# Kernel tuning notes

Hardware: AMD Instinct MI355X
Metric: run time of the kernel (lower is better)

The kernel has to match this reference:

```python
import jax, jax.numpy as jnp
import numpy as np

BOS_IDX = 1


def setup_inputs() -> dict:
    key = jax.random.key(0)
    ks = jax.random.split(key, 12)
    B, T, S, H, L, V = 16, 128, 64, 512, 2, 32000
    s = 0.05
    return {
        "encoder_outputs": jax.random.normal(ks[0], (B, S, H), jnp.float32),
        "encoder_h": jax.random.normal(ks[1], (L, B, H), jnp.float32) * s,
        "encoder_c": jax.random.normal(ks[2], (L, B, H), jnp.float32) * s,
        "target_tensor": jax.random.randint(ks[3], (B, T), 0, V),
        "embedding": jax.random.normal(ks[4], (V, H), jnp.float32) * s,
        "W_ih": jax.random.normal(ks[5], (L, 4 * H, H), jnp.float32) * s,
        "W_hh": jax.random.normal(ks[6], (L, 4 * H, H), jnp.float32) * s,
        "b_ih": jax.random.normal(ks[7], (L, 4 * H), jnp.float32) * s,
        "b_hh": jax.random.normal(ks[8], (L, 4 * H), jnp.float32) * s,
        "W_out": jax.random.normal(ks[9], (V, H), jnp.float32) * s,
        "b_out": jax.random.normal(ks[10], (V,), jnp.float32) * s,
    }


def reference(encoder_outputs, encoder_h, encoder_c, target_tensor,
              embedding, W_ih, W_hh, b_ih, b_hh, W_out, b_out):
    B, T = target_tensor.shape
    L = W_ih.shape[0]
    # Teacher-forced inputs: BOS then target[:, :-1]
    tokens = jnp.concatenate(
        [jnp.full((B, 1), BOS_IDX, dtype=target_tensor.dtype),
         target_tensor[:, :-1]], axis=1)  # [B, T]
    x = jax.nn.relu(embedding[tokens])  # [B, T, H]
    # The original loop resets (h, c) to encoder_states at EVERY step, so all
    # T single-step LSTM cells are independent -> vectorize over T.
    h_last, c_last = [], []
    for l in range(L):
        h0 = encoder_h[l]  # [B, H]
        c0 = encoder_c[l][:, None, :]  # [B, 1, H]
        gates = (jnp.einsum('bth,gh->btg', x, W_ih[l]) + b_ih[l]
                 + (jnp.einsum('bh,gh->bg', h0, W_hh[l]) + b_hh[l])[:, None, :])
        i, f, g, o = jnp.split(gates, 4, axis=-1)  # torch gate order i,f,g,o
        c = jax.nn.sigmoid(f) * c0 + jax.nn.sigmoid(i) * jnp.tanh(g)
        h = jax.nn.sigmoid(o) * jnp.tanh(c)  # [B, T, H]
        h_last.append(h[:, -1, :])
        c_last.append(c[:, -1, :])
        x = h  # input to next layer (dropout=0 / eval)
    logits = jnp.einsum('bth,vh->btv', x, W_out) + b_out  # [B, T, V]
    return logits, (jnp.stack(h_last), jnp.stack(c_last))
```

## Files before the change

### kernel.cpp

```cpp
#include <hip/hip_runtime.h>
#include <hip/hip_bf16.h>

typedef __bf16 bf16_t;
typedef __bf16 bf16x8 __attribute__((ext_vector_type(8)));
typedef __bf16 bf16x4 __attribute__((ext_vector_type(4)));
typedef float f32x4 __attribute__((ext_vector_type(4)));

#define B_ 16
#define T_ 128
#define H_ 512
#define L_ 2
#define V_ 32000
#define G_ 2048
#define M_ 2048

#define BN 128
#define BK 64

__device__ __forceinline__ float sigf(float x) { return 1.f / (1.f + __expf(-x)); }
__device__ __forceinline__ float tanhf_(float x) { return 2.f / (1.f + __expf(-2.f * x)) - 1.f; }


__global__ __launch_bounds__(256) void prep(const float* __restrict__ emb,
                                            const int* __restrict__ target,
                                            const float* __restrict__ enc_h,
                                            const float* __restrict__ W_ih,
                                            const float* __restrict__ W_hh,
                                            const float* __restrict__ b_ih,
                                            const float* __restrict__ b_hh,
                                            const float* __restrict__ W_out,
                                            bf16_t* __restrict__ x,
                                            bf16_t* __restrict__ wih_b,
                                            bf16_t* __restrict__ wout_b,
                                            float* __restrict__ biasall) {
    const int blk = blockIdx.x;
    const int tid = threadIdx.x;
    if (blk < 256) {
        int idx = blk * 256 + tid;
        int b = idx & 15;
        int c = (idx >> 4) & (G_ - 1);
        int l = idx >> 15;
        int gate = (c >> 4) & 3;
        int h = ((c >> 6) << 4) | (c & 15);
        int r = gate * H_ + h;
        const float* hrow = enc_h + ((size_t)l * B_ + b) * H_;
        const float* wrow = W_hh + ((size_t)l * G_ + r) * H_;
        float acc = b_ih[l * G_ + r] + b_hh[l * G_ + r];
        #pragma unroll 4
        for (int k = 0; k < H_; k += 4) {
            float4 hv = *(const float4*)(hrow + k);
            float4 wv = *(const float4*)(wrow + k);
            acc += hv.x * wv.x + hv.y * wv.y + hv.z * wv.z + hv.w * wv.w;
        }
        biasall[((size_t)l * B_ + b) * G_ + c] = acc;
    } else if (blk < 2304) {
        int idx = (blk - 256) * 256 + tid;
        int k4 = idx & 127;
        int c  = (idx >> 7) & (G_ - 1);
        int l  = idx >> 18;
        int gate = (c >> 4) & 3;
        int h = ((c >> 6) << 4) | (c & 15);
        int r = gate * H_ + h;
        float4 v = *(const float4*)(W_ih + ((size_t)l * G_ + r) * H_ + k4 * 4);
        bf16x4 o;
        o[0] = (bf16_t)v.x; o[1] = (bf16_t)v.y; o[2] = (bf16_t)v.z; o[3] = (bf16_t)v.w;
        *(bf16x4*)(wih_b + ((size_t)l * G_ + c) * H_ + k4 * 4) = o;
    } else if (blk < 3328) {
        int idx = (blk - 2304) * 256 + tid;
        int m  = idx >> 7;
        int h4 = (idx & 127) << 2;
        int b = m >> 7, t = m & 127;
        int tok = (t == 0) ? 1 : target[b * T_ + t - 1];
        float4 v = *(const float4*)(emb + (size_t)tok * H_ + h4);
        bf16x4 o;
        o[0] = (bf16_t)fmaxf(v.x, 0.f);
        o[1] = (bf16_t)fmaxf(v.y, 0.f);
        o[2] = (bf16_t)fmaxf(v.z, 0.f);
        o[3] = (bf16_t)fmaxf(v.w, 0.f);
        *(bf16x4*)(x + (size_t)m * H_ + h4) = o;
    } else {
        int idx = (blk - 3328) * 256 + tid;
        float4 v = ((const float4*)W_out)[idx];
        bf16x4 o;
        o[0] = (bf16_t)v.x; o[1] = (bf16_t)v.y; o[2] = (bf16_t)v.z; o[3] = (bf16_t)v.w;
        ((bf16x4*)wout_b)[idx] = o;
    }
}

template<int BMt, int MODE>
__global__ __launch_bounds__(256) void gemm_bt(const bf16_t* __restrict__ A,
                                               const bf16_t* __restrict__ B,
                                               float* __restrict__ C,
                                               const float* __restrict__ bias,
                                               int M, int N, int K,
                                               const float* __restrict__ enc_c,
                                               bf16_t* __restrict__ xout,
                                               float* __restrict__ out_h,
                                               float* __restrict__ out_c,
                                               int l) {
    constexpr int MIc = BMt / 32;
    constexpr int NA  = BMt / 8;
    constexpr int NB  = BN / 8;
    __shared__ __align__(16) bf16_t As[BMt * BK];
    __shared__ __align__(16) bf16_t Bs[BN * BK];

    const int tid  = threadIdx.x;
    const int lane = tid & 63;
    const int wave = tid >> 6;
    const int wm = wave >> 1, wn = wave & 1;
    const int quad = lane >> 4;
    const int r16  = lane & 15;

    const int nwg = gridDim.x;
    const int q  = nwg >> 3;
    const int wg = (blockIdx.x & 7) * q + (blockIdx.x >> 3);
    const int nbx = M / BMt;
    const int bx = wg % nbx;
    const int by = wg / nbx;
    const int tileM = bx * BMt;
    const int tileN = by * BN;

    const int srow = lane >> 3;
    const int scol = (((lane & 7) ^ (lane >> 3)) << 3);

    f32x4 acc[MIc][4];
    #pragma unroll
    for (int i = 0; i < MIc; i++)
        #pragma unroll
        for (int j = 0; j < 4; j++) acc[i][j] = (f32x4){0.f, 0.f, 0.f, 0.f};

    const int nk = K / BK;
    for (int kt = 0; kt < nk; ++kt) {
        const int k0 = kt * BK;
        #pragma unroll
        for (int ii = 0; ii < (NA + NB) / 4; ++ii) {
            const int i = ii * 4 + wave;
            const bf16_t* src;
            bf16_t* dst;
            if (i < NA) {
                const int r0 = i * 8;
                src = A + (size_t)(tileM + r0 + srow) * K + k0 + scol;
                dst = As + r0 * BK;
            } else {
                const int r0 = (i - NA) * 8;
                src = B + (size_t)(tileN + r0 + srow) * K + k0 + scol;
                dst = Bs + r0 * BK;
            }
            __builtin_amdgcn_global_load_lds(
                (const __attribute__((address_space(1))) void*)src,
                (__attribute__((address_space(3))) void*)dst, 16, 0, 0);
        }
        __syncthreads();

        #pragma unroll
        for (int ks = 0; ks < 2; ++ks) {
            bf16x8 af[MIc], bfr[4];
            const int ub = ks * 4 + quad;
            #pragma unroll
            for (int mi = 0; mi < MIc; mi++) {
                const int row = wm * (BMt / 2) + mi * 16 + r16;
                af[mi] = *(const bf16x8*)(As + row * BK + ((ub ^ (r16 & 7)) << 3));
            }
            #pragma unroll
            for (int ni = 0; ni < 4; ni++) {
                const int row = wn * 64 + ni * 16 + r16;
                bfr[ni] = *(const bf16x8*)(Bs + row * BK + ((ub ^ (r16 & 7)) << 3));
            }
            #pragma unroll
            for (int mi = 0; mi < MIc; mi++)
                #pragma unroll
                for (int ni = 0; ni < 4; ni++)
                    acc[mi][ni] = __builtin_amdgcn_mfma_f32_16x16x32_bf16(
                        af[mi], bfr[ni], acc[mi][ni], 0, 0, 0);
        }
        __syncthreads();
    }

    if (MODE == 0) {
        #pragma unroll
        for (int mi = 0; mi < MIc; mi++) {
            #pragma unroll
            for (int ni = 0; ni < 4; ni++) {
                const int col = tileN + wn * 64 + ni * 16 + r16;
                const float bv = bias[col];
                #pragma unroll
                for (int rr = 0; rr < 4; rr++) {
                    const int row = tileM + wm * (BMt / 2) + mi * 16 + quad * 4 + rr;
                    __builtin_nontemporal_store(acc[mi][ni][rr] + bv,
                                                &C[(size_t)row * N + col]);
                }
            }
        }
    } else {
        const int b = tileM >> 7;
        const float* brow = bias + (size_t)b * G_;
        float bv[4];
        #pragma unroll
        for (int g = 0; g < 4; g++)
            bv[g] = brow[tileN + wn * 64 + g * 16 + r16];
        const int h = (2 * by + wn) * 16 + r16;
        const float c0 = enc_c[((size_t)l * B_ + b) * H_ + h];
        #pragma unroll
        for (int mi = 0; mi < MIc; mi++) {
            #pragma unroll
            for (int rr = 0; rr < 4; rr++) {
                const int t = (tileM & 127) + wm * (BMt / 2) + mi * 16 + quad * 4 + rr;
                const float gi = acc[mi][0][rr] + bv[0];
                const float gf = acc[mi][1][rr] + bv[1];
                const float gg = acc[mi][2][rr] + bv[2];
                const float go = acc[mi][3][rr] + bv[3];
                const float c = sigf(gf) * c0 + sigf(gi) * tanhf_(gg);
                const float hv = sigf(go) * tanhf_(c);
                xout[(size_t)(b * T_ + t) * H_ + h] = (bf16_t)hv;
                if (t == T_ - 1) {
                    out_h[((size_t)l * B_ + b) * H_ + h] = hv;
                    out_c[((size_t)l * B_ + b) * H_ + h] = c;
                }
            }
        }
    }
}

extern "C" void kernel_launch(void* const* d_in, const int* in_sizes, int n_in,
                              void* d_out, int out_size, void* d_ws, size_t ws_size,
                              hipStream_t stream) {
    const float* enc_h  = (const float*)d_in[1];
    const float* enc_c  = (const float*)d_in[2];
    const int*   target = (const int*)d_in[3];
    const float* emb    = (const float*)d_in[4];
    const float* W_ih   = (const float*)d_in[5];
    const float* W_hh   = (const float*)d_in[6];
    const float* b_ih   = (const float*)d_in[7];
    const float* b_hh   = (const float*)d_in[8];
    const float* W_out  = (const float*)d_in[9];
    const float* b_out  = (const float*)d_in[10];
    float* out = (float*)d_out;

    char* w = (char*)d_ws;
    bf16_t* x       = (bf16_t*)(w);
    bf16_t* wih_b   = (bf16_t*)(w + 2097152);
    bf16_t* wout_b  = (bf16_t*)(w + 6291456);
    bf16_t* x2      = (bf16_t*)(w + 39059456);
    float*  biasall = (float*)(w + 55836672);

    float* out_h = out + (size_t)M_ * V_;
    float* out_c = out_h + (size_t)L_ * B_ * H_;

    prep<<<19328, 256, 0, stream>>>(emb, target, enc_h, W_ih, W_hh, b_ih, b_hh,
                                    W_out, x, wih_b, wout_b, biasall);

    gemm_bt<64, 1><<<(M_ / 64) * (G_ / BN), 256, 0, stream>>>(
        x, wih_b, nullptr, biasall, M_, G_, H_,
        enc_c, x2, out_h, out_c, 0);
    gemm_bt<64, 1><<<(M_ / 64) * (G_ / BN), 256, 0, stream>>>(
        x2, wih_b + (size_t)G_ * H_, nullptr, biasall + (size_t)B_ * G_,
        M_, G_, H_, enc_c, x, out_h, out_c, 1);

    gemm_bt<128, 0><<<(M_ / 128) * (V_ / BN), 256, 0, stream>>>(
        x, wout_b, out, b_out, M_, V_, H_,
        nullptr, nullptr, nullptr, nullptr, 0);
}
```

Before: 454.4 us.

## Add dedicated pipelined logits GEMM with direct-to-LDS loads and wider W_out cast

Replaces the generic templated GEMM for the large vocabulary projection with a specialized 512-thread kernel that uses 128x256 tiles, triple-buffered LDS fed by global_load_lds async copies, explicit vmcnt waits and barriers, and raised wave priority around the MFMA block. The gate GEMM is split out into its own kernel with the fused LSTM epilogue. The W_out fp32-to-bf16 conversion now handles 8 elements per thread, which cuts the prep grid size. The goal is to overlap global loads with MFMA compute and raise data reuse in the dominant output GEMM, at the cost of more LDS and register use per block and hand-tuned synchronization that is tied to the fixed problem shape.

```diff
diff --git a/kernel.cpp b/kernel.cpp
--- a/kernel.cpp
+++ b/kernel.cpp
@@ -80,24 +80,25 @@
         *(bf16x4*)(x + (size_t)m * H_ + h4) = o;
     } else {
         int idx = (blk - 3328) * 256 + tid;
-        float4 v = ((const float4*)W_out)[idx];
-        bf16x4 o;
-        o[0] = (bf16_t)v.x; o[1] = (bf16_t)v.y; o[2] = (bf16_t)v.z; o[3] = (bf16_t)v.w;
-        ((bf16x4*)wout_b)[idx] = o;
+        const float4* p = (const float4*)W_out + (size_t)idx * 2;
+        float4 v0 = p[0], v1 = p[1];
+        bf16x8 o;
+        o[0] = (bf16_t)v0.x; o[1] = (bf16_t)v0.y; o[2] = (bf16_t)v0.z; o[3] = (bf16_t)v0.w;
+        o[4] = (bf16_t)v1.x; o[5] = (bf16_t)v1.y; o[6] = (bf16_t)v1.z; o[7] = (bf16_t)v1.w;
+        ((bf16x8*)wout_b)[idx] = o;
     }
 }
 
-template<int BMt, int MODE>
-__global__ __launch_bounds__(256) void gemm_bt(const bf16_t* __restrict__ A,
-                                               const bf16_t* __restrict__ B,
-                                               float* __restrict__ C,
-                                               const float* __restrict__ bias,
-                                               int M, int N, int K,
-                                               const float* __restrict__ enc_c,
-                                               bf16_t* __restrict__ xout,
-                                               float* __restrict__ out_h,
-                                               float* __restrict__ out_c,
-                                               int l) {
+template<int BMt>
+__global__ __launch_bounds__(256) void gemm_gates(const bf16_t* __restrict__ A,
+                                                  const bf16_t* __restrict__ B,
+                                                  const float* __restrict__ bias,
+                                                  int M, int N, int K,
+                                                  const float* __restrict__ enc_c,
+                                                  bf16_t* __restrict__ xout,
+                                                  float* __restrict__ out_h,
+                                                  float* __restrict__ out_c,
+                                                  int l) {
     constexpr int MIc = BMt / 32;
     constexpr int NA  = BMt / 8;
     constexpr int NB  = BN / 8;
@@ -176,46 +177,143 @@
         __syncthreads();
     }
 
-    if (MODE == 0) {
-        #pragma unroll
-        for (int mi = 0; mi < MIc; mi++) {
-            #pragma unroll
-            for (int ni = 0; ni < 4; ni++) {
-                const int col = tileN + wn * 64 + ni * 16 + r16;
-                const float bv = bias[col];
+    const int b = tileM >> 7;
+    const float* brow = bias + (size_t)b * G_;
+    float bv[4];
+    #pragma unroll
+    for (int g = 0; g < 4; g++)
+        bv[g] = brow[tileN + wn * 64 + g * 16 + r16];
+    const int h = (2 * by + wn) * 16 + r16;
+    const float c0 = enc_c[((size_t)l * B_ + b) * H_ + h];
+    #pragma unroll
+    for (int mi = 0; mi < MIc; mi++) {
+        #pragma unroll
+        for (int rr = 0; rr < 4; rr++) {
+            const int t = (tileM & 127) + wm * (BMt / 2) + mi * 16 + quad * 4 + rr;
+            const float gi = acc[mi][0][rr] + bv[0];
+            const float gf = acc[mi][1][rr] + bv[1];
+            const float gg = acc[mi][2][rr] + bv[2];
+            const float go = acc[mi][3][rr] + bv[3];
+            const float c = sigf(gf) * c0 + sigf(gi) * tanhf_(gg);
+            const float hv = sigf(go) * tanhf_(c);
+            xout[(size_t)(b * T_ + t) * H_ + h] = (bf16_t)hv;
+            if (t == T_ - 1) {
+                out_h[((size_t)l * B_ + b) * H_ + h] = hv;
+                out_c[((size_t)l * B_ + b) * H_ + h] = c;
+            }
+        }
+    }
+}
+
+#define LBM 128
+#define LBN 256
+#define LBK 64
+#define LNK 8
+__global__ __launch_bounds__(512, 1) void gemm_logits(const bf16_t* __restrict__ A,
+                                                      const bf16_t* __restrict__ B,
+                                                      float* __restrict__ C,
+                                                      const float* __restrict__ bias) {
+    __shared__ __align__(16) bf16_t Abuf[3][LBM * LBK];
+    __shared__ __align__(16) bf16_t Bbuf[3][LBN * LBK];
+
+    const int tid  = threadIdx.x;
+    const int lane = tid & 63;
+    const int wave = tid >> 6;
+    const int wm = wave >> 2, wn = wave & 3;
+    const int quad = lane >> 4;
+    const int r16  = lane & 15;
+
+    const int wg = (blockIdx.x & 7) * 250 + (blockIdx.x >> 3);
+    const int tileM = (wg & 15) * LBM;
+    const int tileN = (wg >> 4) * LBN;
+
+    const int srow = lane >> 3;
+    const int scol = (((lane & 7) ^ srow) << 3);
+
+    f32x4 acc[4][4];
+    #pragma unroll
+    for (int i = 0; i < 4; i++)
+        #pragma unroll
+        for (int j = 0; j < 4; j++) acc[i][j] = (f32x4){0.f, 0.f, 0.f, 0.f};
+
+    auto issue = [&](int t, int buf) {
+        const int k0 = t * LBK;
+        #pragma unroll
+        for (int i = 0; i < 6; ++i) {
+            const int rbase = (i < 2 ? i * 64 : (i - 2) * 64) + wave * 8;
+            if (i < 2) {
+                const bf16_t* src = A + (size_t)(tileM + rbase + srow) * H_ + k0 + scol;
+                __builtin_amdgcn_global_load_lds(
+                    (const __attribute__((address_space(1))) void*)src,
+                    (__attribute__((address_space(3))) void*)(&Abuf[buf][rbase * LBK]),
+                    16, 0, 0);
+            } else {
+                const bf16_t* src = B + (size_t)(tileN + rbase + srow) * H_ + k0 + scol;
+                __builtin_amdgcn_global_load_lds(
+                    (const __attribute__((address_space(1))) void*)src,
+                    (__attribute__((address_space(3))) void*)(&Bbuf[buf][rbase * LBK]),
+                    16, 0, 0);
+            }
+        }
+    };
+
+    issue(0, 0);
+    issue(1, 1);
+    asm volatile("s_waitcnt vmcnt(6)" ::: "memory");
+    __builtin_amdgcn_sched_barrier(0);
+    __builtin_amdgcn_s_barrier();
+    __builtin_amdgcn_sched_barrier(0);
+
+    #pragma unroll
+    for (int j = 0; j < LNK; ++j) {
+        const int jb = j % 3;
+        if (j + 2 < LNK) issue(j + 2, (j + 2) % 3);
+        __builtin_amdgcn_sched_barrier(0);
+
+        bf16x8 af[4][2], bfv[4][2];
+        #pragma unroll
+        for (int ks = 0; ks < 2; ++ks) {
+            const int ub = ks * 4 + quad;
+            const int pu = (ub ^ (r16 & 7)) << 3;
+            #pragma unroll
+            for (int mi = 0; mi < 4; mi++)
+                af[mi][ks] = *(const bf16x8*)(&Abuf[jb][(wm * 64 + mi * 16 + r16) * LBK + pu]);
+            #pragma unroll
+            for (int ni = 0; ni < 4; ni++)
+                bfv[ni][ks] = *(const bf16x8*)(&Bbuf[jb][(wn * 64 + ni * 16 + r16) * LBK + pu]);
+        }
+
+        __builtin_amdgcn_s_setprio(1);
+        #pragma unroll
+        for (int ks = 0; ks < 2; ++ks)
+            #pragma unroll
+            for (int mi = 0; mi < 4; mi++)
                 #pragma unroll
-                for (int rr = 0; rr < 4; rr++) {
-                    const int row = tileM + wm * (BMt / 2) + mi * 16 + quad * 4 + rr;
-                    __builtin_nontemporal_store(acc[mi][ni][rr] + bv,
-                                                &C[(size_t)row * N + col]);
-                }
-            }
-        }
-    } else {
-        const int b = tileM >> 7;
-        const float* brow = bias + (size_t)b * G_;
-        float bv[4];
-        #pragma unroll
-        for (int g = 0; g < 4; g++)
-            bv[g] = brow[tileN + wn * 64 + g * 16 + r16];
-        const int h = (2 * by + wn) * 16 + r16;
-        const float c0 = enc_c[((size_t)l * B_ + b) * H_ + h];
-        #pragma unroll
-        for (int mi = 0; mi < MIc; mi++) {
+                for (int ni = 0; ni < 4; ni++)
+                    acc[mi][ni] = __builtin_amdgcn_mfma_f32_16x16x32_bf16(
+                        af[mi][ks], bfv[ni][ks], acc[mi][ni], 0, 0, 0);
+        __builtin_amdgcn_s_setprio(0);
+
+        if (j < LNK - 1) {
+            if (j < LNK - 2) { asm volatile("s_waitcnt vmcnt(6)" ::: "memory"); }
+            else             { asm volatile("s_waitcnt vmcnt(0)" ::: "memory"); }
+            __builtin_amdgcn_sched_barrier(0);
+            __builtin_amdgcn_s_barrier();
+            __builtin_amdgcn_sched_barrier(0);
+        }
+    }
+
+    #pragma unroll
+    for (int mi = 0; mi < 4; mi++) {
+        #pragma unroll
+        for (int ni = 0; ni < 4; ni++) {
+            const int col = tileN + wn * 64 + ni * 16 + r16;
+            const float bv = bias[col];
             #pragma unroll
             for (int rr = 0; rr < 4; rr++) {
-                const int t = (tileM & 127) + wm * (BMt / 2) + mi * 16 + quad * 4 + rr;
-                const float gi = acc[mi][0][rr] + bv[0];
-                const float gf = acc[mi][1][rr] + bv[1];
-                const float gg = acc[mi][2][rr] + bv[2];
-                const float go = acc[mi][3][rr] + bv[3];
-                const float c = sigf(gf) * c0 + sigf(gi) * tanhf_(gg);
-                const float hv = sigf(go) * tanhf_(c);
-                xout[(size_t)(b * T_ + t) * H_ + h] = (bf16_t)hv;
-                if (t == T_ - 1) {
-                    out_h[((size_t)l * B_ + b) * H_ + h] = hv;
-                    out_c[((size_t)l * B_ + b) * H_ + h] = c;
-                }
+                const int row = tileM + wm * 64 + mi * 16 + quad * 4 + rr;
+                __builtin_nontemporal_store(acc[mi][ni][rr] + bv,
+                                            &C[(size_t)row * V_ + col]);
             }
         }
     }
@@ -246,17 +344,15 @@
     float* out_h = out + (size_t)M_ * V_;
     float* out_c = out_h + (size_t)L_ * B_ * H_;
 
-    prep<<<19328, 256, 0, stream>>>(emb, target, enc_h, W_ih, W_hh, b_ih, b_hh,
+    prep<<<11328, 256, 0, stream>>>(emb, target, enc_h, W_ih, W_hh, b_ih, b_hh,
                                     W_out, x, wih_b, wout_b, biasall);
 
-    gemm_bt<64, 1><<<(M_ / 64) * (G_ / BN), 256, 0, stream>>>(
-        x, wih_b, nullptr, biasall, M_, G_, H_,
+    gemm_gates<64><<<(M_ / 64) * (G_ / BN), 256, 0, stream>>>(
+        x, wih_b, biasall, M_, G_, H_,
         enc_c, x2, out_h, out_c, 0);
-    gemm_bt<64, 1><<<(M_ / 64) * (G_ / BN), 256, 0, stream>>>(
-        x2, wih_b + (size_t)G_ * H_, nullptr, biasall + (size_t)B_ * G_,
+    gemm_gates<64><<<(M_ / 64) * (G_ / BN), 256, 0, stream>>>(
+        x2, wih_b + (size_t)G_ * H_, biasall + (size_t)B_ * G_,
         M_, G_, H_, enc_c, x, out_h, out_c, 1);
 
-    gemm_bt<128, 0><<<(M_ / 128) * (V_ / BN), 256, 0, stream>>>(
-        x, wout_b, out, b_out, M_, V_, H_,
-        nullptr, nullptr, nullptr, nullptr, 0);
+    gemm_logits<<<(M_ / LBM) * (V_ / LBN), 512, 0, stream>>>(x, wout_b, out, b_out);
 }
```

After: 468.5 us. +3.1%, slower.
